# Kernel tuning notes

Measured on AMD Instinct MI355X. Metric: run time of the kernel, lower is better.

## Reference

```python
import jax, jax.numpy as jnp
import numpy as np

BN_EPS = 1e-5


def setup_inputs() -> dict:
    key = jax.random.key(0)
    ks = jax.random.split(key, 8)
    B, C, H, W = 8, 256, 64, 64
    Cqk = C // 8  # query/key channels = out_channels // 8
    x = jax.random.normal(ks[0], (B, C, H, W), dtype=jnp.float32)
    # 1x1 convs == per-pixel matmuls; kaiming-normal-ish scale
    wq = jax.random.normal(ks[1], (Cqk, C), dtype=jnp.float32) * np.sqrt(2.0 / C)
    bq = jnp.zeros((Cqk,), dtype=jnp.float32)
    wk = jax.random.normal(ks[2], (Cqk, C), dtype=jnp.float32) * np.sqrt(2.0 / C)
    bk = jnp.zeros((Cqk,), dtype=jnp.float32)
    wv = jax.random.normal(ks[3], (C, C), dtype=jnp.float32) * np.sqrt(2.0 / C)
    bv = jnp.zeros((C,), dtype=jnp.float32)
    # gamma is initialized to 0 in the original; use a small nonzero value so
    # the attention path actually contributes (and has nontrivial gradients)
    gamma = jnp.full((1,), 0.5, dtype=jnp.float32)
    bn_weight = jnp.ones((C,), dtype=jnp.float32)
    bn_bias = jnp.zeros((C,), dtype=jnp.float32)
    return {"x": x, "wq": wq, "bq": bq, "wk": wk, "bk": bk,
            "wv": wv, "bv": bv, "gamma": gamma,
            "bn_weight": bn_weight, "bn_bias": bn_bias}


def reference(x, wq, bq, wk, bk, wv, bv, gamma, bn_weight, bn_bias):
    B, C, H, W = x.shape
    N = H * W
    xf = x.reshape(B, C, N)  # (B, C, N)
    # 1x1 conv projections as channel matmuls
    q = jnp.einsum('oc,bcn->bno', wq, xf) + bq            # (B, N, Cqk)
    k = jnp.einsum('oc,bcn->bon', wk, xf) + bk[:, None]   # (B, Cqk, N)
    v = jnp.einsum('oc,bcn->bon', wv, xf) + bv[:, None]   # (B, C, N)
    # attention[b, i, j] = softmax_j(q_i . k_j)  -- full N x N matrix
    scores = jnp.einsum('bno,bom->bnm', q, k)             # (B, N, N)
    attn = jax.nn.softmax(scores, axis=2)
    # out[b, c, i] = sum_j v[b, c, j] * attn[b, i, j]
    out = jnp.einsum('bcj,bij->bci', v, attn)             # (B, C, N)
    out = out.reshape(B, C, H, W)
    out = gamma[0] * out + x
    # BatchNorm2d in training mode: batch statistics over (B, H, W)
    mean = jnp.mean(out, axis=(0, 2, 3), keepdims=True)
    var = jnp.var(out, axis=(0, 2, 3), keepdims=True)
    out = (out - mean) * jax.lax.rsqrt(var + BN_EPS)
    out = out * bn_weight[None, :, None, None] + bn_bias[None, :, None, None]
    return jax.nn.relu(out)
```

## Files before the change

### kernel.cpp

```cpp
#include <hip/hip_runtime.h>
#include <stdint.h>

#define B_ 8
#define C_ 256
#define N_ 4096
#define CQK 32

typedef __attribute__((ext_vector_type(8))) _Float16 f16x8;
typedef __attribute__((ext_vector_type(4))) float f32x4;

__device__ __forceinline__ unsigned short f2bf_rne(float f) {
  unsigned u = __builtin_bit_cast(unsigned, f);
  u += 0x7FFFu + ((u >> 16) & 1u);
  return (unsigned short)(u >> 16);
}

__global__ __launch_bounds__(256) void xpose_kernel(
    const float* __restrict__ x, _Float16* __restrict__ xT)
{
  __shared__ float xs[64 * 129];
  const int t  = threadIdx.x;
  const int blk = blockIdx.x;
  const int nt = blk & 31;
  const int ct = (blk >> 5) & 3;
  const int b  = blk >> 7;
  const int c0 = ct * 64, n0 = nt * 128;

  #pragma unroll
  for (int p = 0; p < 8; ++p) {
    int cc = p * 8 + (t >> 5);
    int nn = (t & 31) * 4;
    float4 v = *(const float4*)(x + ((size_t)(b * C_ + c0 + cc)) * N_ + n0 + nn);
    xs[cc * 129 + nn]     = v.x;
    xs[cc * 129 + nn + 1] = v.y;
    xs[cc * 129 + nn + 2] = v.z;
    xs[cc * 129 + nn + 3] = v.w;
  }
  __syncthreads();
  #pragma unroll
  for (int p = 0; p < 4; ++p) {
    int id = p * 256 + t;
    int cchunk = id & 7, n = id >> 3;
    _Float16 h[8];
    #pragma unroll
    for (int j = 0; j < 8; ++j) h[j] = (_Float16)xs[(cchunk * 8 + j) * 129 + n];
    *(f16x8*)(xT + ((size_t)(b * N_) + n0 + n) * C_ + c0 + cchunk * 8) = *(f16x8*)h;
  }
}

__global__ __launch_bounds__(256) void wconv_kernel(
    const float* __restrict__ wq, const float* __restrict__ wk,
    const float* __restrict__ wv, _Float16* __restrict__ wf)
{
  int idx = blockIdx.x * 256 + threadIdx.x;
  int e = idx * 4;
  int o = e >> 8, c = e & 255;
  const float* src;
  if (o < 32)      src = wq + o * 256 + c;
  else if (o < 64) src = wk + (o - 32) * 256 + c;
  else             src = wv + (o - 64) * 256 + c;
  float4 v = *(const float4*)src;
  _Float16 h[4] = {(_Float16)v.x, (_Float16)v.y, (_Float16)v.z, (_Float16)v.w};
  *(uint2*)(wf + e) = *(uint2*)h;
}

__global__ __launch_bounds__(256, 4) void proj_gemm_kernel(
    const _Float16* __restrict__ xT, const _Float16* __restrict__ wf,
    const float* __restrict__ bq, const float* __restrict__ bk,
    const float* __restrict__ bv,
    _Float16* __restrict__ qf, _Float16* __restrict__ kf,
    _Float16* __restrict__ vout)
{
  const int t = threadIdx.x, lane = t & 63;
  const int w = t >> 6;
  const int l15 = lane & 15, q4 = lane >> 4;
  const int blk = blockIdx.x;
  const int otile = blk % 5;
  const int nt = blk / 5;
  const int b  = nt >> 5;
  const int n0 = (nt & 31) * 128;
  const int o0w = (w & 1) * 32;
  const int n0w = (w >> 1) * 64;

  f32x4 acc[2][4];
  const f32x4 zf = {0.f, 0.f, 0.f, 0.f};
  #pragma unroll
  for (int a = 0; a < 2; ++a)
    #pragma unroll
    for (int bb = 0; bb < 4; ++bb) acc[a][bb] = zf;

  const _Float16* wbase = wf + (size_t)(otile * 64 + o0w) * 256;
  const _Float16* xbase = xT + ((size_t)(b * N_) + n0 + n0w) * C_;

  #pragma unroll
  for (int kc = 0; kc < 8; ++kc) {
    f16x8 af[2], bfr[4];
    #pragma unroll
    for (int ob = 0; ob < 2; ++ob)
      af[ob] = *(const f16x8*)(wbase + (ob * 16 + l15) * 256 + kc * 32 + q4 * 8);
    #pragma unroll
    for (int nb = 0; nb < 4; ++nb)
      bfr[nb] = *(const f16x8*)(xbase + (nb * 16 + l15) * 256 + kc * 32 + q4 * 8);
    #pragma unroll
    for (int ob = 0; ob < 2; ++ob)
      #pragma unroll
      for (int nb = 0; nb < 4; ++nb)
        acc[ob][nb] = __builtin_amdgcn_mfma_f32_16x16x32_f16(af[ob], bfr[nb], acc[ob][nb], 0, 0, 0);
  }

  if (otile == 0) {
    _Float16* dst = (o0w == 0) ? qf : kf;
    const float* bias = (o0w == 0) ? bq : bk;
    #pragma unroll
    for (int ob = 0; ob < 2; ++ob) {
      float4 b4 = *(const float4*)(bias + ob * 16 + q4 * 4);
      #pragma unroll
      for (int nb = 0; nb < 4; ++nb) {
        int pixel = n0 + n0w + nb * 16 + l15;
        _Float16 h[4];
        h[0] = (_Float16)(acc[ob][nb][0] + b4.x);
        h[1] = (_Float16)(acc[ob][nb][1] + b4.y);
        h[2] = (_Float16)(acc[ob][nb][2] + b4.z);
        h[3] = (_Float16)(acc[ob][nb][3] + b4.w);
        *(uint2*)(dst + ((size_t)(b * N_) + pixel) * CQK + ob * 16 + q4 * 4) = *(uint2*)h;
      }
    }
  } else {
    int cbase = (otile - 1) * 64 + o0w;
    #pragma unroll
    for (int ob = 0; ob < 2; ++ob) {
      float4 b4 = *(const float4*)(bv + cbase + ob * 16 + q4 * 4);
      #pragma unroll
      for (int nb = 0; nb < 4; ++nb) {
        int pixel = n0 + n0w + nb * 16 + l15;
        #pragma unroll
        for (int r = 0; r < 4; ++r) {
          int c = cbase + ob * 16 + q4 * 4 + r;
          float bval = (r == 0) ? b4.x : (r == 1) ? b4.y : (r == 2) ? b4.z : b4.w;
          vout[((size_t)(b * C_) + c) * N_ + pixel] = (_Float16)(acc[ob][nb][r] + bval);
        }
      }
    }
  }
}

__global__ __launch_bounds__(512, 4) void attn_kernel(
    const float* __restrict__ x, const float* __restrict__ gptr,
    const _Float16* __restrict__ qf, const _Float16* __restrict__ kf,
    const _Float16* __restrict__ vf, unsigned short* __restrict__ yout)
{
  __shared__ __align__(16) char smem[10768];
  _Float16* Plds  = (_Float16*)smem;
  float* pmax   = (float*)(smem + 9216);
  float* psum   = (float*)(smem + 9728);
  float* alphal = (float*)(smem + 10240);
  float* lrowl  = (float*)(smem + 10496);
  int*   flagl  = (int*)(smem + 10752);

  const int t = threadIdx.x, lane = t & 63;
  const int w = t >> 6;
  const int l15 = lane & 15, q4 = lane >> 4;
  const int b  = blockIdx.x & 7;
  const int it = blockIdx.x >> 3;
  const int i0 = it * 64;
  const int qg = w >> 1, jh = w & 1;
  const int row = qg * 16 + l15;
  const float gamma = gptr[0];

  const f16x8 qfr = *(const f16x8*)(qf + ((size_t)(b * N_) + i0 + qg * 16 + l15) * CQK + q4 * 8);

  f32x4 acc[2][4];
  const f32x4 zf = {0.f, 0.f, 0.f, 0.f};
  #pragma unroll
  for (int a = 0; a < 2; ++a)
    #pragma unroll
    for (int bb = 0; bb < 4; ++bb) acc[a][bb] = zf;

  float mold = -1e30f, lrun = 0.f;

  for (int jt = 0; jt < N_ / 64; ++jt) {
    const int jbase = jt * 64;

    f16x8 kfr[2];
    #pragma unroll
    for (int jbb = 0; jbb < 2; ++jbb) {
      int j = jbase + (jh * 2 + jbb) * 16 + l15;
      kfr[jbb] = *(const f16x8*)(kf + ((size_t)(b * N_) + j) * CQK + q4 * 8);
    }
    f16x8 vfr[2][2];
    #pragma unroll
    for (int ks = 0; ks < 2; ++ks)
      #pragma unroll
      for (int cb = 0; cb < 2; ++cb)
        vfr[ks][cb] = *(const f16x8*)(vf + ((size_t)(b * C_) + w * 32 + cb * 16 + l15) * N_ + jbase + ks * 32 + q4 * 8);

    f32x4 sv[2];
    #pragma unroll
    for (int jbb = 0; jbb < 2; ++jbb)
      sv[jbb] = __builtin_amdgcn_mfma_f32_16x16x32_f16(kfr[jbb], qfr, zf, 0, 0, 0);

    float lm = fmaxf(fmaxf(fmaxf(sv[0][0], sv[0][1]), fmaxf(sv[0][2], sv[0][3])),
                     fmaxf(fmaxf(sv[1][0], sv[1][1]), fmaxf(sv[1][2], sv[1][3])));
    lm = fmaxf(lm, __shfl_xor(lm, 16));
    lm = fmaxf(lm, __shfl_xor(lm, 32));
    if (lane < 16) pmax[jh * 64 + qg * 16 + lane] = lm;
    __syncthreads();

    float mnew = fmaxf(mold, fmaxf(pmax[row], pmax[64 + row]));
    bool upd = mnew > mold;
    float alpha = __expf(mold - mnew);
    float p[2][4];
    float ts = 0.f;
    #pragma unroll
    for (int jbb = 0; jbb < 2; ++jbb)
      #pragma unroll
      for (int r = 0; r < 4; ++r) {
        float pv = __expf(sv[jbb][r] - mnew);
        p[jbb][r] = pv; ts += pv;
      }
    ts += __shfl_xor(ts, 16);
    ts += __shfl_xor(ts, 32);
    if (lane < 16) psum[jh * 64 + qg * 16 + lane] = ts;
    if (jh == 0 && lane < 16) alphal[qg * 16 + lane] = alpha;
    {
      char* pb = (char*)Plds + (qg * 16 + l15) * 144 + jh * 64 + q4 * 8;
      #pragma unroll
      for (int jbb = 0; jbb < 2; ++jbb) {
        _Float16 h[4];
        h[0] = (_Float16)p[jbb][0];
        h[1] = (_Float16)p[jbb][1];
        h[2] = (_Float16)p[jbb][2];
        h[3] = (_Float16)p[jbb][3];
        *(uint2*)(pb + jbb * 32) = *(uint2*)h;
      }
    }
    if (__ballot(upd) != 0ull) { if (lane == 0) flagl[jt & 1] = 1; }
    if (t == 0) flagl[(jt + 1) & 1] = 0;
    mold = mnew;
    __syncthreads();

    lrun = lrun * alpha + psum[row] + psum[64 + row];

    if (flagl[jt & 1]) {
      #pragma unroll
      for (int ib = 0; ib < 4; ++ib) {
        float av = alphal[ib * 16 + l15];
        #pragma unroll
        for (int cb = 0; cb < 2; ++cb)
          #pragma unroll
          for (int r = 0; r < 4; ++r) acc[cb][ib][r] *= av;
      }
    }
    #pragma unroll
    for (int ks = 0; ks < 2; ++ks) {
      f16x8 pf[4];
      #pragma unroll
      for (int ib = 0; ib < 4; ++ib)
        pf[ib] = *(const f16x8*)((char*)Plds + (ib * 16 + l15) * 144 + ks * 64 + q4 * 16);
      #pragma unroll
      for (int cb = 0; cb < 2; ++cb)
        #pragma unroll
        for (int ib = 0; ib < 4; ++ib)
          acc[cb][ib] = __builtin_amdgcn_mfma_f32_16x16x32_f16(vfr[ks][cb], pf[ib], acc[cb][ib], 0, 0, 0);
    }
  }

  if (jh == 0 && lane < 16) lrowl[qg * 16 + lane] = lrun;
  __syncthreads();
  #pragma unroll
  for (int ib = 0; ib < 4; ++ib) {
    float linv = 1.0f / lrowl[ib * 16 + l15];
    int i = i0 + ib * 16 + l15;
    #pragma unroll
    for (int cb = 0; cb < 2; ++cb) {
      #pragma unroll
      for (int r = 0; r < 4; ++r) {
        int c = w * 32 + cb * 16 + q4 * 4 + r;
        size_t off = ((size_t)(b * C_) + c) * N_ + i;
        float o = acc[cb][ib][r] * linv;
        yout[off] = f2bf_rne(fmaf(gamma, o, x[off]));
      }
    }
  }
}

__global__ __launch_bounds__(256) void bnstats_kernel(
    const unsigned short* __restrict__ y, float* __restrict__ meanw, float* __restrict__ rstdw)
{
  const int c = blockIdx.x;
  const int t = threadIdx.x;
  float s1 = 0.f, s2 = 0.f;
  for (int b = 0; b < B_; ++b) {
    const unsigned short* p = y + ((size_t)(b * C_ + c)) * N_;
    #pragma unroll
    for (int r = 0; r < 2; ++r) {
      uint4 u = *(const uint4*)(p + r * 2048 + t * 8);
      unsigned uu[4] = {u.x, u.y, u.z, u.w};
      #pragma unroll
      for (int k = 0; k < 4; ++k) {
        float a = __builtin_bit_cast(float, uu[k] << 16);
        float bb = __builtin_bit_cast(float, uu[k] & 0xFFFF0000u);
        s1 += a + bb;
        s2 += a * a + bb * bb;
      }
    }
  }
  __shared__ float r1[256], r2[256];
  r1[t] = s1; r2[t] = s2;
  __syncthreads();
  for (int s = 128; s > 0; s >>= 1) {
    if (t < s) { r1[t] += r1[t + s]; r2[t] += r2[t + s]; }
    __syncthreads();
  }
  if (t == 0) {
    float mean = r1[0] * (1.0f / 32768.0f);
    float var  = r2[0] * (1.0f / 32768.0f) - mean * mean;
    meanw[c] = mean;
    rstdw[c] = rsqrtf(var + 1e-5f);
  }
}

__global__ __launch_bounds__(256) void bnapply_kernel(
    const unsigned short* __restrict__ y, float* __restrict__ out,
    const float* __restrict__ meanw, const float* __restrict__ rstdw,
    const float* __restrict__ bnw, const float* __restrict__ bnb)
{
  size_t idx = (size_t)blockIdx.x * 256 + threadIdx.x;
  size_t el = idx * 8;
  int c = (int)((el >> 12) & 255);
  float sc = bnw[c] * rstdw[c];
  float sh = fmaf(-meanw[c], sc, bnb[c]);
  uint4 u = *(const uint4*)(y + el);
  unsigned uu[4] = {u.x, u.y, u.z, u.w};
  float4 o0, o1;
  float v[8];
  #pragma unroll
  for (int k = 0; k < 4; ++k) {
    v[2 * k]     = __builtin_bit_cast(float, uu[k] << 16);
    v[2 * k + 1] = __builtin_bit_cast(float, uu[k] & 0xFFFF0000u);
  }
  o0.x = fmaxf(fmaf(v[0], sc, sh), 0.f);
  o0.y = fmaxf(fmaf(v[1], sc, sh), 0.f);
  o0.z = fmaxf(fmaf(v[2], sc, sh), 0.f);
  o0.w = fmaxf(fmaf(v[3], sc, sh), 0.f);
  o1.x = fmaxf(fmaf(v[4], sc, sh), 0.f);
  o1.y = fmaxf(fmaf(v[5], sc, sh), 0.f);
  o1.z = fmaxf(fmaf(v[6], sc, sh), 0.f);
  o1.w = fmaxf(fmaf(v[7], sc, sh), 0.f);
  *(float4*)(out + el) = o0;
  *(float4*)(out + el + 4) = o1;
}

extern "C" void kernel_launch(void* const* d_in, const int* in_sizes, int n_in,
                              void* d_out, int out_size, void* d_ws, size_t ws_size,
                              hipStream_t stream)
{
  const float* x   = (const float*)d_in[0];
  const float* wq  = (const float*)d_in[1];
  const float* bq  = (const float*)d_in[2];
  const float* wk  = (const float*)d_in[3];
  const float* bk  = (const float*)d_in[4];
  const float* wv  = (const float*)d_in[5];
  const float* bv  = (const float*)d_in[6];
  const float* gm  = (const float*)d_in[7];
  const float* bnw = (const float*)d_in[8];
  const float* bnb = (const float*)d_in[9];
  float* out = (float*)d_out;

  _Float16* xT  = (_Float16*)d_out;
  _Float16* vfp = (_Float16*)((char*)d_out + (size_t)B_ * C_ * N_ * 2);

  char* ws = (char*)d_ws;
  _Float16* qf = (_Float16*)(ws);
  _Float16* kf = (_Float16*)(ws + ((size_t)2 << 20));
  unsigned short* yout = (unsigned short*)(ws + ((size_t)4 << 20));
  _Float16* wf = (_Float16*)(ws + ((size_t)21 << 20));
  float* meanw = (float*)(ws + ((size_t)22 << 20));
  float* rstdw = (float*)(ws + ((size_t)22 << 20) + 4096);

  hipLaunchKernelGGL(xpose_kernel, dim3(1024), dim3(256), 0, stream, x, xT);
  hipLaunchKernelGGL(wconv_kernel, dim3(80), dim3(256), 0, stream, wq, wk, wv, wf);
  hipLaunchKernelGGL(proj_gemm_kernel, dim3(1280), dim3(256), 0, stream,
                     xT, wf, bq, bk, bv, qf, kf, vfp);
  hipLaunchKernelGGL(attn_kernel, dim3(512), dim3(512), 0, stream,
                     x, gm, qf, kf, vfp, yout);
  hipLaunchKernelGGL(bnstats_kernel, dim3(256), dim3(256), 0, stream,
                     yout, meanw, rstdw);
  hipLaunchKernelGGL(bnapply_kernel, dim3(4096), dim3(256), 0, stream,
                     yout, out, meanw, rstdw, bnw, bnb);
}
```

Before: 298.1 us.

## Restructure attention so each wave owns full query rows, drop block syncs

The attention kernel is reorganized so each wave handles 16 query rows across all 64 keys per tile and all 256 value channels, removing cross-wave max/sum exchange and both __syncthreads per iteration. Keys are prefetched one tile ahead, log2e is folded into q so exp2 is used directly, and P is packed with cvt_pkrtz. The intermediate y is now stored as fp32 in the output buffer and BN apply runs in place, while bnstats uses wave shuffles with 1024 threads. In exchange, the accumulator count grows to 16 tiles per wave, which raises register pressure and halves the grid to 256 blocks. V is also reloaded per wave from global memory rather than shared across waves.

```diff
diff --git a/kernel.cpp b/kernel.cpp
--- a/kernel.cpp
+++ b/kernel.cpp
@@ -7,13 +7,10 @@
 #define CQK 32
 
 typedef __attribute__((ext_vector_type(8))) _Float16 f16x8;
+typedef __attribute__((ext_vector_type(2))) _Float16 f16x2;
 typedef __attribute__((ext_vector_type(4))) float f32x4;
 
-__device__ __forceinline__ unsigned short f2bf_rne(float f) {
-  unsigned u = __builtin_bit_cast(unsigned, f);
-  u += 0x7FFFu + ((u >> 16) & 1u);
-  return (unsigned short)(u >> 16);
-}
+#define LOG2E 1.4426950408889634f
 
 __global__ __launch_bounds__(256) void xpose_kernel(
     const float* __restrict__ x, _Float16* __restrict__ xT)
@@ -111,6 +108,7 @@
   if (otile == 0) {
     _Float16* dst = (o0w == 0) ? qf : kf;
     const float* bias = (o0w == 0) ? bq : bk;
+    const float scl = (o0w == 0) ? LOG2E : 1.0f;
     #pragma unroll
     for (int ob = 0; ob < 2; ++ob) {
       float4 b4 = *(const float4*)(bias + ob * 16 + q4 * 4);
@@ -118,10 +116,10 @@
       for (int nb = 0; nb < 4; ++nb) {
         int pixel = n0 + n0w + nb * 16 + l15;
         _Float16 h[4];
-        h[0] = (_Float16)(acc[ob][nb][0] + b4.x);
-        h[1] = (_Float16)(acc[ob][nb][1] + b4.y);
-        h[2] = (_Float16)(acc[ob][nb][2] + b4.z);
-        h[3] = (_Float16)(acc[ob][nb][3] + b4.w);
+        h[0] = (_Float16)((acc[ob][nb][0] + b4.x) * scl);
+        h[1] = (_Float16)((acc[ob][nb][1] + b4.y) * scl);
+        h[2] = (_Float16)((acc[ob][nb][2] + b4.z) * scl);
+        h[3] = (_Float16)((acc[ob][nb][3] + b4.w) * scl);
         *(uint2*)(dst + ((size_t)(b * N_) + pixel) * CQK + ob * 16 + q4 * 4) = *(uint2*)h;
       }
     }
@@ -144,184 +142,149 @@
   }
 }
 
-__global__ __launch_bounds__(512, 4) void attn_kernel(
+__global__ __launch_bounds__(512, 2) void attn_kernel(
     const float* __restrict__ x, const float* __restrict__ gptr,
     const _Float16* __restrict__ qf, const _Float16* __restrict__ kf,
-    const _Float16* __restrict__ vf, unsigned short* __restrict__ yout)
-{
-  __shared__ __align__(16) char smem[10768];
-  _Float16* Plds  = (_Float16*)smem;
-  float* pmax   = (float*)(smem + 9216);
-  float* psum   = (float*)(smem + 9728);
-  float* alphal = (float*)(smem + 10240);
-  float* lrowl  = (float*)(smem + 10496);
-  int*   flagl  = (int*)(smem + 10752);
-
+    const _Float16* __restrict__ vf, float* __restrict__ yout)
+{
+  __shared__ __align__(16) char smem[8 * 2304];
   const int t = threadIdx.x, lane = t & 63;
   const int w = t >> 6;
   const int l15 = lane & 15, q4 = lane >> 4;
   const int b  = blockIdx.x & 7;
-  const int it = blockIdx.x >> 3;
-  const int i0 = it * 64;
-  const int qg = w >> 1, jh = w & 1;
-  const int row = qg * 16 + l15;
-  const float gamma = gptr[0];
-
-  const f16x8 qfr = *(const f16x8*)(qf + ((size_t)(b * N_) + i0 + qg * 16 + l15) * CQK + q4 * 8);
-
-  f32x4 acc[2][4];
+  const int i0 = (blockIdx.x >> 3) * 128;
+  const int myrow = w * 16;
+  char* Pw = smem + w * 2304;
+
+  const f16x8 qfr = *(const f16x8*)(qf + ((size_t)(b * N_) + i0 + myrow + l15) * CQK + q4 * 8);
+
+  const _Float16* kb = kf + (size_t)b * N_ * CQK;
+  const _Float16* vb = vf + (size_t)b * C_ * N_;
+
+  f32x4 acc[16];
   const f32x4 zf = {0.f, 0.f, 0.f, 0.f};
   #pragma unroll
-  for (int a = 0; a < 2; ++a)
-    #pragma unroll
-    for (int bb = 0; bb < 4; ++bb) acc[a][bb] = zf;
+  for (int ct = 0; ct < 16; ++ct) acc[ct] = zf;
 
   float mold = -1e30f, lrun = 0.f;
+
+  f16x8 kcur[4];
+  #pragma unroll
+  for (int jb = 0; jb < 4; ++jb)
+    kcur[jb] = *(const f16x8*)(kb + (size_t)(jb * 16 + l15) * CQK + q4 * 8);
 
   for (int jt = 0; jt < N_ / 64; ++jt) {
     const int jbase = jt * 64;
 
-    f16x8 kfr[2];
-    #pragma unroll
-    for (int jbb = 0; jbb < 2; ++jbb) {
-      int j = jbase + (jh * 2 + jbb) * 16 + l15;
-      kfr[jbb] = *(const f16x8*)(kf + ((size_t)(b * N_) + j) * CQK + q4 * 8);
-    }
-    f16x8 vfr[2][2];
-    #pragma unroll
-    for (int ks = 0; ks < 2; ++ks)
-      #pragma unroll
-      for (int cb = 0; cb < 2; ++cb)
-        vfr[ks][cb] = *(const f16x8*)(vf + ((size_t)(b * C_) + w * 32 + cb * 16 + l15) * N_ + jbase + ks * 32 + q4 * 8);
-
-    f32x4 sv[2];
-    #pragma unroll
-    for (int jbb = 0; jbb < 2; ++jbb)
-      sv[jbb] = __builtin_amdgcn_mfma_f32_16x16x32_f16(kfr[jbb], qfr, zf, 0, 0, 0);
+    f32x4 sv[4];
+    #pragma unroll
+    for (int jb = 0; jb < 4; ++jb)
+      sv[jb] = __builtin_amdgcn_mfma_f32_16x16x32_f16(kcur[jb], qfr, zf, 0, 0, 0);
+
+    const int jnext = (jt == N_ / 64 - 1) ? 0 : jbase + 64;
+    #pragma unroll
+    for (int jb = 0; jb < 4; ++jb)
+      kcur[jb] = *(const f16x8*)(kb + (size_t)(jnext + jb * 16 + l15) * CQK + q4 * 8);
 
     float lm = fmaxf(fmaxf(fmaxf(sv[0][0], sv[0][1]), fmaxf(sv[0][2], sv[0][3])),
                      fmaxf(fmaxf(sv[1][0], sv[1][1]), fmaxf(sv[1][2], sv[1][3])));
+    lm = fmaxf(lm, fmaxf(fmaxf(fmaxf(sv[2][0], sv[2][1]), fmaxf(sv[2][2], sv[2][3])),
+                         fmaxf(fmaxf(sv[3][0], sv[3][1]), fmaxf(sv[3][2], sv[3][3]))));
     lm = fmaxf(lm, __shfl_xor(lm, 16));
     lm = fmaxf(lm, __shfl_xor(lm, 32));
-    if (lane < 16) pmax[jh * 64 + qg * 16 + lane] = lm;
-    __syncthreads();
-
-    float mnew = fmaxf(mold, fmaxf(pmax[row], pmax[64 + row]));
+    float mnew = fmaxf(mold, lm);
     bool upd = mnew > mold;
-    float alpha = __expf(mold - mnew);
-    float p[2][4];
+    float alpha = __builtin_amdgcn_exp2f(mold - mnew);
+
+    float p[4][4];
     float ts = 0.f;
     #pragma unroll
-    for (int jbb = 0; jbb < 2; ++jbb)
+    for (int jb = 0; jb < 4; ++jb)
       #pragma unroll
       for (int r = 0; r < 4; ++r) {
-        float pv = __expf(sv[jbb][r] - mnew);
-        p[jbb][r] = pv; ts += pv;
+        float pv = __builtin_amdgcn_exp2f(sv[jb][r] - mnew);
+        p[jb][r] = pv; ts += pv;
       }
     ts += __shfl_xor(ts, 16);
     ts += __shfl_xor(ts, 32);
-    if (lane < 16) psum[jh * 64 + qg * 16 + lane] = ts;
-    if (jh == 0 && lane < 16) alphal[qg * 16 + lane] = alpha;
-    {
-      char* pb = (char*)Plds + (qg * 16 + l15) * 144 + jh * 64 + q4 * 8;
-      #pragma unroll
-      for (int jbb = 0; jbb < 2; ++jbb) {
-        _Float16 h[4];
-        h[0] = (_Float16)p[jbb][0];
-        h[1] = (_Float16)p[jbb][1];
-        h[2] = (_Float16)p[jbb][2];
-        h[3] = (_Float16)p[jbb][3];
-        *(uint2*)(pb + jbb * 32) = *(uint2*)h;
+    lrun = lrun * alpha + ts;
+    mold = mnew;
+
+    #pragma unroll
+    for (int jb = 0; jb < 4; ++jb) {
+      uint2 pk;
+      pk.x = __builtin_bit_cast(unsigned, __builtin_amdgcn_cvt_pkrtz(p[jb][0], p[jb][1]));
+      pk.y = __builtin_bit_cast(unsigned, __builtin_amdgcn_cvt_pkrtz(p[jb][2], p[jb][3]));
+      *(uint2*)(Pw + l15 * 144 + jb * 32 + q4 * 8) = pk;
+    }
+
+    if (__any(upd)) {
+      #pragma unroll
+      for (int ct = 0; ct < 16; ++ct)
+        #pragma unroll
+        for (int r = 0; r < 4; ++r) acc[ct][r] *= alpha;
+    }
+
+    #pragma unroll
+    for (int ks = 0; ks < 2; ++ks) {
+      f16x8 pf = *(const f16x8*)(Pw + l15 * 144 + ks * 64 + q4 * 16);
+      #pragma unroll
+      for (int ct = 0; ct < 16; ++ct) {
+        f16x8 vfr = *(const f16x8*)(vb + (size_t)(ct * 16 + l15) * N_ + jbase + ks * 32 + q4 * 8);
+        acc[ct] = __builtin_amdgcn_mfma_f32_16x16x32_f16(vfr, pf, acc[ct], 0, 0, 0);
       }
     }
-    if (__ballot(upd) != 0ull) { if (lane == 0) flagl[jt & 1] = 1; }
-    if (t == 0) flagl[(jt + 1) & 1] = 0;
-    mold = mnew;
-    __syncthreads();
-
-    lrun = lrun * alpha + psum[row] + psum[64 + row];
-
-    if (flagl[jt & 1]) {
-      #pragma unroll
-      for (int ib = 0; ib < 4; ++ib) {
-        float av = alphal[ib * 16 + l15];
-        #pragma unroll
-        for (int cb = 0; cb < 2; ++cb)
-          #pragma unroll
-          for (int r = 0; r < 4; ++r) acc[cb][ib][r] *= av;
-      }
-    }
-    #pragma unroll
-    for (int ks = 0; ks < 2; ++ks) {
-      f16x8 pf[4];
-      #pragma unroll
-      for (int ib = 0; ib < 4; ++ib)
-        pf[ib] = *(const f16x8*)((char*)Plds + (ib * 16 + l15) * 144 + ks * 64 + q4 * 16);
-      #pragma unroll
-      for (int cb = 0; cb < 2; ++cb)
-        #pragma unroll
-        for (int ib = 0; ib < 4; ++ib)
-          acc[cb][ib] = __builtin_amdgcn_mfma_f32_16x16x32_f16(vfr[ks][cb], pf[ib], acc[cb][ib], 0, 0, 0);
-    }
-  }
-
-  if (jh == 0 && lane < 16) lrowl[qg * 16 + lane] = lrun;
-  __syncthreads();
-  #pragma unroll
-  for (int ib = 0; ib < 4; ++ib) {
-    float linv = 1.0f / lrowl[ib * 16 + l15];
-    int i = i0 + ib * 16 + l15;
-    #pragma unroll
-    for (int cb = 0; cb < 2; ++cb) {
-      #pragma unroll
-      for (int r = 0; r < 4; ++r) {
-        int c = w * 32 + cb * 16 + q4 * 4 + r;
-        size_t off = ((size_t)(b * C_) + c) * N_ + i;
-        float o = acc[cb][ib][r] * linv;
-        yout[off] = f2bf_rne(fmaf(gamma, o, x[off]));
-      }
-    }
-  }
-}
-
-__global__ __launch_bounds__(256) void bnstats_kernel(
-    const unsigned short* __restrict__ y, float* __restrict__ meanw, float* __restrict__ rstdw)
+  }
+
+  const float gamma = gptr[0];
+  float linv = 1.0f / lrun;
+  const int i = i0 + myrow + l15;
+  #pragma unroll
+  for (int ct = 0; ct < 16; ++ct) {
+    #pragma unroll
+    for (int r = 0; r < 4; ++r) {
+      int c = ct * 16 + q4 * 4 + r;
+      size_t off = ((size_t)(b * C_) + c) * N_ + i;
+      float o = acc[ct][r] * linv;
+      yout[off] = fmaf(gamma, o, x[off]);
+    }
+  }
+}
+
+__global__ __launch_bounds__(1024) void bnstats_kernel(
+    const float* __restrict__ y, float* __restrict__ meanw, float* __restrict__ rstdw)
 {
   const int c = blockIdx.x;
   const int t = threadIdx.x;
   float s1 = 0.f, s2 = 0.f;
+  #pragma unroll
   for (int b = 0; b < B_; ++b) {
-    const unsigned short* p = y + ((size_t)(b * C_ + c)) * N_;
-    #pragma unroll
-    for (int r = 0; r < 2; ++r) {
-      uint4 u = *(const uint4*)(p + r * 2048 + t * 8);
-      unsigned uu[4] = {u.x, u.y, u.z, u.w};
-      #pragma unroll
-      for (int k = 0; k < 4; ++k) {
-        float a = __builtin_bit_cast(float, uu[k] << 16);
-        float bb = __builtin_bit_cast(float, uu[k] & 0xFFFF0000u);
-        s1 += a + bb;
-        s2 += a * a + bb * bb;
-      }
-    }
-  }
-  __shared__ float r1[256], r2[256];
-  r1[t] = s1; r2[t] = s2;
+    float4 v = *(const float4*)(y + ((size_t)(b * C_ + c)) * N_ + t * 4);
+    s1 += v.x + v.y + v.z + v.w;
+    s2 += v.x * v.x + v.y * v.y + v.z * v.z + v.w * v.w;
+  }
+  #pragma unroll
+  for (int off = 1; off < 64; off <<= 1) {
+    s1 += __shfl_xor(s1, off);
+    s2 += __shfl_xor(s2, off);
+  }
+  __shared__ float r1[16], r2[16];
+  const int wid = t >> 6;
+  if ((t & 63) == 0) { r1[wid] = s1; r2[wid] = s2; }
   __syncthreads();
-  for (int s = 128; s > 0; s >>= 1) {
-    if (t < s) { r1[t] += r1[t + s]; r2[t] += r2[t + s]; }
-    __syncthreads();
-  }
   if (t == 0) {
-    float mean = r1[0] * (1.0f / 32768.0f);
-    float var  = r2[0] * (1.0f / 32768.0f) - mean * mean;
+    float a1 = 0.f, a2 = 0.f;
+    #pragma unroll
+    for (int k = 0; k < 16; ++k) { a1 += r1[k]; a2 += r2[k]; }
+    float mean = a1 * (1.0f / 32768.0f);
+    float var  = a2 * (1.0f / 32768.0f) - mean * mean;
     meanw[c] = mean;
     rstdw[c] = rsqrtf(var + 1e-5f);
   }
 }
 
 __global__ __launch_bounds__(256) void bnapply_kernel(
-    const unsigned short* __restrict__ y, float* __restrict__ out,
+    float* __restrict__ y,
     const float* __restrict__ meanw, const float* __restrict__ rstdw,
     const float* __restrict__ bnw, const float* __restrict__ bnb)
 {
@@ -330,25 +293,18 @@
   int c = (int)((el >> 12) & 255);
   float sc = bnw[c] * rstdw[c];
   float sh = fmaf(-meanw[c], sc, bnb[c]);
-  uint4 u = *(const uint4*)(y + el);
-  unsigned uu[4] = {u.x, u.y, u.z, u.w};
-  float4 o0, o1;
-  float v[8];
-  #pragma unroll
-  for (int k = 0; k < 4; ++k) {
-    v[2 * k]     = __builtin_bit_cast(float, uu[k] << 16);
-    v[2 * k + 1] = __builtin_bit_cast(float, uu[k] & 0xFFFF0000u);
-  }
-  o0.x = fmaxf(fmaf(v[0], sc, sh), 0.f);
-  o0.y = fmaxf(fmaf(v[1], sc, sh), 0.f);
-  o0.z = fmaxf(fmaf(v[2], sc, sh), 0.f);
-  o0.w = fmaxf(fmaf(v[3], sc, sh), 0.f);
-  o1.x = fmaxf(fmaf(v[4], sc, sh), 0.f);
-  o1.y = fmaxf(fmaf(v[5], sc, sh), 0.f);
-  o1.z = fmaxf(fmaf(v[6], sc, sh), 0.f);
-  o1.w = fmaxf(fmaf(v[7], sc, sh), 0.f);
-  *(float4*)(out + el) = o0;
-  *(float4*)(out + el + 4) = o1;
+  float4 v0 = *(const float4*)(y + el);
+  float4 v1 = *(const float4*)(y + el + 4);
+  v0.x = fmaxf(fmaf(v0.x, sc, sh), 0.f);
+  v0.y = fmaxf(fmaf(v0.y, sc, sh), 0.f);
+  v0.z = fmaxf(fmaf(v0.z, sc, sh), 0.f);
+  v0.w = fmaxf(fmaf(v0.w, sc, sh), 0.f);
+  v1.x = fmaxf(fmaf(v1.x, sc, sh), 0.f);
+  v1.y = fmaxf(fmaf(v1.y, sc, sh), 0.f);
+  v1.z = fmaxf(fmaf(v1.z, sc, sh), 0.f);
+  v1.w = fmaxf(fmaf(v1.w, sc, sh), 0.f);
+  *(float4*)(y + el) = v0;
+  *(float4*)(y + el + 4) = v1;
 }
 
 extern "C" void kernel_launch(void* const* d_in, const int* in_sizes, int n_in,
@@ -360,32 +316,31 @@
   const float* bq  = (const float*)d_in[2];
   const float* wk  = (const float*)d_in[3];
   const float* bk  = (const float*)d_in[4];
+  const float* bv  = (const float*)d_in[6];
   const float* wv  = (const float*)d_in[5];
-  const float* bv  = (const float*)d_in[6];
   const float* gm  = (const float*)d_in[7];
   const float* bnw = (const float*)d_in[8];
   const float* bnb = (const float*)d_in[9];
-  float* out = (float*)d_out;
-
-  _Float16* xT  = (_Float16*)d_out;
-  _Float16* vfp = (_Float16*)((char*)d_out + (size_t)B_ * C_ * N_ * 2);
+
+  _Float16* xT = (_Float16*)d_out;
+  float* y = (float*)d_out;
 
   char* ws = (char*)d_ws;
-  _Float16* qf = (_Float16*)(ws);
-  _Float16* kf = (_Float16*)(ws + ((size_t)2 << 20));
-  unsigned short* yout = (unsigned short*)(ws + ((size_t)4 << 20));
-  _Float16* wf = (_Float16*)(ws + ((size_t)21 << 20));
-  float* meanw = (float*)(ws + ((size_t)22 << 20));
-  float* rstdw = (float*)(ws + ((size_t)22 << 20) + 4096);
+  _Float16* qf  = (_Float16*)(ws);
+  _Float16* kf  = (_Float16*)(ws + ((size_t)2 << 20));
+  _Float16* vfp = (_Float16*)(ws + ((size_t)4 << 20));
+  _Float16* wf  = (_Float16*)(ws + ((size_t)21 << 20));
+  float* meanw  = (float*)(ws + ((size_t)22 << 20));
+  float* rstdw  = (float*)(ws + ((size_t)22 << 20) + 4096);
 
   hipLaunchKernelGGL(xpose_kernel, dim3(1024), dim3(256), 0, stream, x, xT);
   hipLaunchKernelGGL(wconv_kernel, dim3(80), dim3(256), 0, stream, wq, wk, wv, wf);
   hipLaunchKernelGGL(proj_gemm_kernel, dim3(1280), dim3(256), 0, stream,
                      xT, wf, bq, bk, bv, qf, kf, vfp);
-  hipLaunchKernelGGL(attn_kernel, dim3(512), dim3(512), 0, stream,
-                     x, gm, qf, kf, vfp, yout);
-  hipLaunchKernelGGL(bnstats_kernel, dim3(256), dim3(256), 0, stream,
-                     yout, meanw, rstdw);
+  hipLaunchKernelGGL(attn_kernel, dim3(256), dim3(512), 0, stream,
+                     x, gm, qf, kf, vfp, y);
+  hipLaunchKernelGGL(bnstats_kernel, dim3(256), dim3(1024), 0, stream,
+                     y, meanw, rstdw);
   hipLaunchKernelGGL(bnapply_kernel, dim3(4096), dim3(256), 0, stream,
-                     yout, out, meanw, rstdw, bnw, bnb);
-}
+                     y, meanw, rstdw, bnw, bnb);
+}
```

New measurement: 631.5 us. 2.12x slower.
